# Performance work log

Measured on AMD Instinct MI355X. Metric: run time of the kernel, lower is better.

The kernel has to match this reference:

```python
import jax, jax.numpy as jnp
import numpy as np

N_QUBITS = 12
N_LAYERS = 3


def _apply_ry(state, theta, q):
    # state: (2,)*n real statevector; RY on qubit q
    c = jnp.cos(theta * 0.5)
    s = jnp.sin(theta * 0.5)
    st = jnp.moveaxis(state, q, 0)
    st = jnp.stack([c * st[0] - s * st[1], s * st[0] + c * st[1]])
    return jnp.moveaxis(st, 0, q)


def _apply_cz(state, q, r):
    st = jnp.moveaxis(state, (q, r), (0, 1))
    st = st.at[1, 1].multiply(-1.0)
    return jnp.moveaxis(st, (0, 1), (q, r))


def _embed(x, params):
    # angle-embedding ansatz: L layers of RY(theta[l,q]+x[q]) + CZ ring
    n = N_QUBITS
    state = jnp.zeros((2,) * n, dtype=x.dtype).at[(0,) * n].set(1.0)
    for l in range(N_LAYERS):
        for q in range(n):
            state = _apply_ry(state, params[l, q] + x[q], q)
        for q in range(n):
            state = _apply_cz(state, q, (q + 1) % n)
    return state.reshape(-1)  # (2^n,)


def setup_inputs() -> dict:
    key = jax.random.key(0)
    k1, k2, k3 = jax.random.split(key, 3)
    data = jax.random.uniform(k1, (2048, N_QUBITS), dtype=jnp.float32)
    labels = jax.random.randint(k2, (2048,), 0, 2, dtype=jnp.int32)
    params = jax.random.normal(k3, (N_LAYERS, N_QUBITS), dtype=jnp.float32)
    return {"data": data, "labels": labels, "params": params}


def reference(data, labels, params):
    # Psi[i] = U(x_i, params)|0>, k_ij = |<psi_j|psi_i>|^2 (== prob of amp 0 of U^dag(x_j)U(x_i)|0>)
    psi = jax.vmap(_embed, in_axes=(0, None))(data, params)  # (N, 2^n)
    K = jnp.square(psi @ psi.T)                              # (N, N) pairwise kernel
    lab = 2.0 * labels.astype(psi.dtype) - 1.0               # {0,1} -> {-1,+1}
    LL = jnp.outer(lab, lab)
    kernel_polarity = jnp.sum(LL * K)
    square_sum_k = jnp.sum(K * K)
    square_sum_l = jnp.sum(LL * LL)
    return kernel_polarity / jnp.sqrt(square_sum_k * square_sum_l)
```

## Files before the change

### kernel.cpp

```cpp
#include <hip/hip_runtime.h>
#include <math.h>

#define NQ    12
#define DIM   4096
#define K_EXT 8192
#define KSL   1024
#define NSAMP 2048
#define NLAY  3
#define NT2   16
#define NTRI2 136
#define NSLICE 8
#define BK    64

typedef __attribute__((ext_vector_type(8)))  short bf16x8;
typedef __attribute__((ext_vector_type(16))) float floatx16;

__device__ __forceinline__ unsigned short f32_to_bf16(float x) {
    unsigned u = __builtin_bit_cast(unsigned, x);
    u += 0x7FFFu + ((u >> 16) & 1u);
    return (unsigned short)(u >> 16);
}
__device__ __forceinline__ float bf16_to_f32(unsigned short h) {
    unsigned u = (unsigned)h << 16;
    return __builtin_bit_cast(float, u);
}

__device__ __forceinline__ void gl_lds16(const unsigned short* g, unsigned short* l) {
    __builtin_amdgcn_global_load_lds(
        (const __attribute__((address_space(1))) unsigned int*)g,
        (__attribute__((address_space(3))) unsigned int*)l,
        16, 0, 0);
}

__device__ __forceinline__ void tri_decode(int bid, int& bi, int& bj) {
    int i = (int)((33.0 - sqrt(33.0*33.0 - 8.0*(double)bid)) * 0.5);
    int start = i*(33-i)/2;
    while (bid < start)               { --i; start = i*(33-i)/2; }
    while (bid >= start + (NT2 - i))  { start += NT2 - i; ++i; }
    bi = i; bj = i + (bid - start);
}

__global__ __launch_bounds__(256) void sim_kernel(const float* __restrict__ data,
                                                  const float* __restrict__ params,
                                                  unsigned short* __restrict__ pe)
{
    __shared__ float CS[2*36], SN[2*36];
    __shared__ float ex[2][128*33];
    const int tid  = threadIdx.x;
    const int wave = tid >> 6, lane = tid & 63;
    const int sidx = wave >> 1;
    const int w    = wave & 1;
    const int smp  = blockIdx.x * 2 + sidx;

    if (w == 0 && lane < NLAY*NQ) {
        const int q = lane % NQ;
        const float th = 0.5f * (params[lane] + data[smp*NQ + q]);
        CS[sidx*36 + lane] = cosf(th);
        SN[sidx*36 + lane] = sinf(th);
    }
    __syncthreads();

    float v[32];
    #pragma unroll
    for (int r = 0; r < 32; ++r) v[r] = 0.f;
    if (w == 0 && lane == 0) v[0] = 1.f;

    const int P5 = __popc(lane & (lane >> 1) & 0x1F) & 1;
    const int l0 = lane & 1, l5 = (lane >> 5) & 1;
    const int base = P5 ^ (l5 & w);
    const float fA0 = base             ? -1.f : 1.f;
    const float fA1 = (base ^ w)       ? -1.f : 1.f;
    const float fB0 = (base ^ l0)      ? -1.f : 1.f;
    const float fB1 = (base ^ l0 ^ w)  ? -1.f : 1.f;

    float*       exw = &ex[sidx][(w*64       + lane)*33];
    const float* exp_ = &ex[sidx][((1-w)*64  + lane)*33];

    #pragma unroll 1
    for (int l = 0; l < NLAY; ++l) {
        const float* cs = &CS[sidx*36 + l*NQ];
        const float* sn = &SN[sidx*36 + l*NQ];
        #pragma unroll
        for (int b = 0; b < 5; ++b) {
            const float c = cs[b], s = sn[b];
            const int M = 1 << b;
            #pragma unroll
            for (int r = 0; r < 32; ++r) {
                if (!(r & M)) {
                    const float a0 = v[r], a1 = v[r | M];
                    v[r]     = c * a0 - s * a1;
                    v[r | M] = s * a0 + c * a1;
                }
            }
        }
        {
            const float c0 = cs[5], s0 = sn[5];
            const float t0 = (lane & 1) ? s0 : -s0;
            #pragma unroll
            for (int r = 0; r < 32; ++r) {
                const int iv = __builtin_bit_cast(int, v[r]);
                const int pv = __builtin_amdgcn_update_dpp(0, iv, 0xB1, 0xF, 0xF, true);
                v[r] = c0 * v[r] + t0 * __builtin_bit_cast(float, pv);
            }
            const float c1 = cs[6], s1 = sn[6];
            const float t1 = (lane & 2) ? s1 : -s1;
            #pragma unroll
            for (int r = 0; r < 32; ++r) {
                const int iv = __builtin_bit_cast(int, v[r]);
                const int pv = __builtin_amdgcn_update_dpp(0, iv, 0x4E, 0xF, 0xF, true);
                v[r] = c1 * v[r] + t1 * __builtin_bit_cast(float, pv);
            }
        }
        #pragma unroll 1
        for (int q = 7; q < 11; ++q) {
            const float c = cs[q], s = sn[q];
            const int   lb = q - 5;
            const float t = ((lane >> lb) & 1) ? s : -s;
            const int   m = 1 << lb;
            #pragma unroll
            for (int r = 0; r < 32; ++r) {
                const float p = __shfl_xor(v[r], m, 64);
                v[r] = c * v[r] + t * p;
            }
        }
        {
            const float c = cs[11], s = sn[11];
            const float t = w ? s : -s;
            __syncthreads();
            #pragma unroll
            for (int r = 0; r < 32; ++r) exw[r] = v[r];
            __syncthreads();
            #pragma unroll
            for (int r = 0; r < 32; ++r) v[r] = c * v[r] + t * exp_[r];
        }
        #pragma unroll
        for (int r = 0; r < 32; ++r) {
            const int P4 = __popc(r & (r >> 1) & 0xF) & 1;
            const int r0 = r & 1, r4 = (r >> 4) & 1;
            float f = r4 ? (r0 ? fB1 : fB0) : (r0 ? fA1 : fA0);
            if (P4) f = -f;
            v[r] *= f;
        }
    }

    const int sw = smp & 7;
    const int ell = w*64 + lane;
    unsigned short* outb = pe + (size_t)smp * K_EXT;
    #pragma unroll
    for (int c = 0; c < 4; ++c) {
        uint4 H, L;
        {
            const float x0 = v[c*8+0], x1 = v[c*8+1];
            const unsigned short h0 = f32_to_bf16(x0), h1 = f32_to_bf16(x1);
            H.x = (unsigned)h0 | ((unsigned)h1 << 16);
            L.x = (unsigned)f32_to_bf16(x0 - bf16_to_f32(h0)) |
                  ((unsigned)f32_to_bf16(x1 - bf16_to_f32(h1)) << 16);
        }
        {
            const float x0 = v[c*8+2], x1 = v[c*8+3];
            const unsigned short h0 = f32_to_bf16(x0), h1 = f32_to_bf16(x1);
            H.y = (unsigned)h0 | ((unsigned)h1 << 16);
            L.y = (unsigned)f32_to_bf16(x0 - bf16_to_f32(h0)) |
                  ((unsigned)f32_to_bf16(x1 - bf16_to_f32(h1)) << 16);
        }
        {
            const float x0 = v[c*8+4], x1 = v[c*8+5];
            const unsigned short h0 = f32_to_bf16(x0), h1 = f32_to_bf16(x1);
            H.z = (unsigned)h0 | ((unsigned)h1 << 16);
            L.z = (unsigned)f32_to_bf16(x0 - bf16_to_f32(h0)) |
                  ((unsigned)f32_to_bf16(x1 - bf16_to_f32(h1)) << 16);
        }
        {
            const float x0 = v[c*8+6], x1 = v[c*8+7];
            const unsigned short h0 = f32_to_bf16(x0), h1 = f32_to_bf16(x1);
            H.w = (unsigned)h0 | ((unsigned)h1 << 16);
            L.w = (unsigned)f32_to_bf16(x0 - bf16_to_f32(h0)) |
                  ((unsigned)f32_to_bf16(x1 - bf16_to_f32(h1)) << 16);
        }
        const int gc  = 4*ell + c;
        const int pos = (gc & ~7) | ((gc ^ sw) & 7);
        *(uint4*)&outb[pos*8]       = H;
        *(uint4*)&outb[DIM + pos*8] = L;
    }
}

__global__ __launch_bounds__(256) void gram_partial(const unsigned short* __restrict__ pe,
                                                    float* __restrict__ Gp)
{
    __shared__ __align__(16) unsigned short stage[2*128*64];

    unsigned short* As = stage;
    unsigned short* Bs = stage + 128*64;

    const int tid   = threadIdx.x;
    const int tile  = blockIdx.x >> 3;
    const int slice = blockIdx.x & 7;
    int bi, bj; tri_decode(tile, bi, bj);
    const int k0 = slice * KSL;

    const int wave = tid >> 6, lane = tid & 63;
    const int qr = (wave >> 1) * 64;
    const int qc = (wave &  1) * 64;
    const int mrow = lane & 31;
    const int chsel = lane >> 5;
    const int sw = mrow & 7;

    floatx16 c00, c01, c10, c11;
    #pragma unroll
    for (int i = 0; i < 16; ++i) { c00[i]=0.f; c01[i]=0.f; c10[i]=0.f; c11[i]=0.f; }

    const int mat  = wave >> 1;
    const int half = wave & 1;
    const unsigned short* gbase = pe
        + ((size_t)((mat ? bj : bi)*128 + half*64 + (lane >> 3))) * K_EXT
        + k0 + (lane & 7)*8;
    unsigned short* lbase = (mat ? Bs : As) + half*64*64;

    for (int kk = 0; kk < KSL; kk += BK) {
        __syncthreads();
        const unsigned short* g = gbase + kk;
        #pragma unroll
        for (int i = 0; i < 8; ++i)
            gl_lds16(g + (size_t)i*8*K_EXT, lbase + i*512);
        __syncthreads();

        #pragma unroll
        for (int ks = 0; ks < 4; ++ks) {
            const int ch = (ks*2 + chsel) ^ sw;
            const bf16x8 a0 = *(const bf16x8*)&As[(qr +      mrow)*64 + ch*8];
            const bf16x8 a1 = *(const bf16x8*)&As[(qr + 32 + mrow)*64 + ch*8];
            const bf16x8 b0 = *(const bf16x8*)&Bs[(qc +      mrow)*64 + ch*8];
            const bf16x8 b1 = *(const bf16x8*)&Bs[(qc + 32 + mrow)*64 + ch*8];
            c00 = __builtin_amdgcn_mfma_f32_32x32x16_bf16(a0, b0, c00, 0, 0, 0);
            c01 = __builtin_amdgcn_mfma_f32_32x32x16_bf16(a0, b1, c01, 0, 0, 0);
            c10 = __builtin_amdgcn_mfma_f32_32x32x16_bf16(a1, b0, c10, 0, 0, 0);
            c11 = __builtin_amdgcn_mfma_f32_32x32x16_bf16(a1, b1, c11, 0, 0, 0);
        }
    }

    float* Gt = Gp + ((size_t)slice * NTRI2 + tile) * 16384;
    const int crow = chsel * 4;
    const int ccol = lane & 31;
    #pragma unroll
    for (int rr = 0; rr < 16; ++rr) {
        const int rl = (rr & 3) + 8*(rr >> 2) + crow;
        const int r0 = qr + rl,  r1 = qr + 32 + rl;
        const int cA = qc + ccol, cB = qc + 32 + ccol;
        Gt[r0*128 + cA] = c00[rr];
        Gt[r0*128 + cB] = c01[rr];
        Gt[r1*128 + cA] = c10[rr];
        Gt[r1*128 + cB] = c11[rr];
    }
}

__global__ __launch_bounds__(256) void gram_reduce(const float* __restrict__ Gp,
                                                   const int* __restrict__ labels,
                                                   double* __restrict__ part1,
                                                   double* __restrict__ part2)
{
    __shared__ float la[128], lb[128];
    __shared__ double red[256];
    const int tid  = threadIdx.x;
    const int tile = blockIdx.x >> 2;
    const int quar = blockIdx.x & 3;
    int bi, bj; tri_decode(tile, bi, bj);

    if (tid < 128) la[tid]       = 2.0f*(float)labels[bi*128 + tid]       - 1.0f;
    else           lb[tid - 128] = 2.0f*(float)labels[bj*128 + tid - 128] - 1.0f;
    __syncthreads();

    const size_t stride = (size_t)NTRI2 * 16384;
    const float* g0 = Gp + (size_t)tile * 16384 + quar * 4096;

    double s1 = 0.0, s2 = 0.0;
    #pragma unroll 2
    for (int u = 0; u < 16; ++u) {
        const int e  = u*256 + tid;
        const int ge = quar*4096 + e;
        float g = 0.f;
        #pragma unroll
        for (int s = 0; s < NSLICE; ++s) g += g0[e + (size_t)s*stride];
        const int row = ge >> 7, col = ge & 127;
        const float w = (bi < bj) ? 2.0f : ((row < col) ? 2.0f : ((row == col) ? 1.0f : 0.0f));
        const float g2 = g * g;
        s1 += (double)(w * la[row] * lb[col] * g2);
        const double d = (double)g2;
        s2 += (double)w * d * d;
    }

    red[tid] = s1; __syncthreads();
    for (int off = 128; off; off >>= 1) { if (tid < off) red[tid] += red[tid+off]; __syncthreads(); }
    if (tid == 0) part1[blockIdx.x] = red[0];
    __syncthreads();
    red[tid] = s2; __syncthreads();
    for (int off = 128; off; off >>= 1) { if (tid < off) red[tid] += red[tid+off]; __syncthreads(); }
    if (tid == 0) part2[blockIdx.x] = red[0];
}

__global__ __launch_bounds__(256) void finalize_kernel(const double* __restrict__ part1,
                                                       const double* __restrict__ part2,
                                                       float* __restrict__ out)
{
    __shared__ double r1[256], r2[256];
    const int tid = threadIdx.x;
    double a = 0.0, b = 0.0;
    #pragma unroll
    for (int u = 0; u < 3; ++u) {
        const int s = tid + u*256;
        if (s < NTRI2*4) { a += part1[s]; b += part2[s]; }
    }
    r1[tid] = a; r2[tid] = b; __syncthreads();
    for (int off = 128; off; off >>= 1) {
        if (tid < off) { r1[tid] += r1[tid+off]; r2[tid] += r2[tid+off]; }
        __syncthreads();
    }
    if (tid == 0) out[0] = (float)(r1[0] / (sqrt(r2[0]) * (double)NSAMP));
}

extern "C" void kernel_launch(void* const* d_in, const int* in_sizes, int n_in,
                              void* d_out, int out_size, void* d_ws, size_t ws_size,
                              hipStream_t stream)
{
    const float* data   = (const float*)d_in[0];
    const int*   labels = (const int*)d_in[1];
    const float* params = (const float*)d_in[2];

    double* part1 = (double*)d_ws;
    double* part2 = part1 + 768;
    unsigned short* psi_ext = (unsigned short*)((char*)d_ws + 16384);
    float* Gp = (float*)((char*)d_ws + 16384 + (size_t)NSAMP*K_EXT*2);

    sim_kernel<<<NSAMP/2, 256, 0, stream>>>(data, params, psi_ext);
    gram_partial<<<NTRI2*NSLICE, 256, 0, stream>>>(psi_ext, Gp);
    gram_reduce<<<NTRI2*4, 256, 0, stream>>>(Gp, labels, part1, part2);
    finalize_kernel<<<1, 256, 0, stream>>>(part1, part2, (float*)d_out);
}
```

Baseline: 154.9 us.

## Replace shuffle gates with LDS transpose alternating register/lane qubit mapping

Each layer now applies five qubits in registers, two via DPP, then does one shared-memory transpose so another five qubits become register-local, instead of four cross-lane shuffles per element plus an exchange for qubit 11. The qubit-to-register mapping alternates between even and odd layers, and the CZ phase is computed per element from popcount parity and applied via sign-bit XOR. This targets the cost of the many ds_bpermute shuffles, in exchange for a larger LDS buffer and the risk of bank conflicts or mapping errors in the final layout used by the store.

```diff
diff --git a/kernel.cpp b/kernel.cpp
--- a/kernel.cpp
+++ b/kernel.cpp
@@ -45,7 +45,7 @@
                                                   unsigned short* __restrict__ pe)
 {
     __shared__ float CS[2*36], SN[2*36];
-    __shared__ float ex[2][128*33];
+    __shared__ float trans[2][4608];
     const int tid  = threadIdx.x;
     const int wave = tid >> 6, lane = tid & 63;
     const int sidx = wave >> 1;
@@ -65,36 +65,34 @@
     for (int r = 0; r < 32; ++r) v[r] = 0.f;
     if (w == 0 && lane == 0) v[0] = 1.f;
 
-    const int P5 = __popc(lane & (lane >> 1) & 0x1F) & 1;
-    const int l0 = lane & 1, l5 = (lane >> 5) & 1;
-    const int base = P5 ^ (l5 & w);
-    const float fA0 = base             ? -1.f : 1.f;
-    const float fA1 = (base ^ w)       ? -1.f : 1.f;
-    const float fB0 = (base ^ l0)      ? -1.f : 1.f;
-    const float fB1 = (base ^ l0 ^ w)  ? -1.f : 1.f;
-
-    float*       exw = &ex[sidx][(w*64       + lane)*33];
-    const float* exp_ = &ex[sidx][((1-w)*64  + lane)*33];
+    float* buf = trans[sidx];
+    float* wb  = buf + 36*lane + 2304*w;
+    const float* rb = buf + ((lane>>2)&15) + 16*w + 36*(lane&3);
 
     #pragma unroll 1
     for (int l = 0; l < NLAY; ++l) {
         const float* cs = &CS[sidx*36 + l*NQ];
         const float* sn = &SN[sidx*36 + l*NQ];
-        #pragma unroll
-        for (int b = 0; b < 5; ++b) {
-            const float c = cs[b], s = sn[b];
-            const int M = 1 << b;
-            #pragma unroll
-            for (int r = 0; r < 32; ++r) {
-                if (!(r & M)) {
-                    const float a0 = v[r], a1 = v[r | M];
-                    v[r]     = c * a0 - s * a1;
-                    v[r | M] = s * a0 + c * a1;
+        const int even = !(l & 1);
+
+        {
+            const int qb = even ? 7 : 2;
+            #pragma unroll
+            for (int b = 0; b < 5; ++b) {
+                const float c = cs[qb + b], s = sn[qb + b];
+                const int M = 1 << b;
+                #pragma unroll
+                for (int r = 0; r < 32; ++r) {
+                    if (!(r & M)) {
+                        const float a0 = v[r], a1 = v[r | M];
+                        v[r]     = c * a0 - s * a1;
+                        v[r | M] = s * a0 + c * a1;
+                    }
                 }
             }
         }
         {
-            const float c0 = cs[5], s0 = sn[5];
+            const float c0 = cs[0], s0 = sn[0];
             const float t0 = (lane & 1) ? s0 : -s0;
             #pragma unroll
             for (int r = 0; r < 32; ++r) {
@@ -102,7 +100,7 @@
                 const int pv = __builtin_amdgcn_update_dpp(0, iv, 0xB1, 0xF, 0xF, true);
                 v[r] = c0 * v[r] + t0 * __builtin_bit_cast(float, pv);
             }
-            const float c1 = cs[6], s1 = sn[6];
+            const float c1 = cs[1], s1 = sn[1];
             const float t1 = (lane & 2) ? s1 : -s1;
             #pragma unroll
             for (int r = 0; r < 32; ++r) {
@@ -111,35 +109,45 @@
                 v[r] = c1 * v[r] + t1 * __builtin_bit_cast(float, pv);
             }
         }
-        #pragma unroll 1
-        for (int q = 7; q < 11; ++q) {
-            const float c = cs[q], s = sn[q];
-            const int   lb = q - 5;
-            const float t = ((lane >> lb) & 1) ? s : -s;
-            const int   m = 1 << lb;
+        __syncthreads();
+        #pragma unroll
+        for (int t = 0; t < 8; ++t) {
+            float4 q4;
+            q4.x = v[4*t]; q4.y = v[4*t+1]; q4.z = v[4*t+2]; q4.w = v[4*t+3];
+            *(float4*)&wb[4*t] = q4;
+        }
+        __syncthreads();
+        #pragma unroll
+        for (int r = 0; r < 32; ++r)
+            v[r] = rb[144*(r & 15) + 2304*(r >> 4)];
+
+        {
+            const int qb = even ? 2 : 7;
+            #pragma unroll
+            for (int b = 0; b < 5; ++b) {
+                const float c = cs[qb + b], s = sn[qb + b];
+                const int M = 1 << b;
+                #pragma unroll
+                for (int r = 0; r < 32; ++r) {
+                    if (!(r & M)) {
+                        const float a0 = v[r], a1 = v[r | M];
+                        v[r]     = c * a0 - s * a1;
+                        v[r | M] = s * a0 + c * a1;
+                    }
+                }
+            }
+        }
+        {
+            const int Base = even ? ((lane & 3) | (((lane >> 2) & 15) << 7) | (w << 11))
+                                  : (lane | (w << 6));
+            const int shift = even ? 2 : 7;
             #pragma unroll
             for (int r = 0; r < 32; ++r) {
-                const float p = __shfl_xor(v[r], m, 64);
-                v[r] = c * v[r] + t * p;
-            }
-        }
-        {
-            const float c = cs[11], s = sn[11];
-            const float t = w ? s : -s;
-            __syncthreads();
-            #pragma unroll
-            for (int r = 0; r < 32; ++r) exw[r] = v[r];
-            __syncthreads();
-            #pragma unroll
-            for (int r = 0; r < 32; ++r) v[r] = c * v[r] + t * exp_[r];
-        }
-        #pragma unroll
-        for (int r = 0; r < 32; ++r) {
-            const int P4 = __popc(r & (r >> 1) & 0xF) & 1;
-            const int r0 = r & 1, r4 = (r >> 4) & 1;
-            float f = r4 ? (r0 ? fB1 : fB0) : (r0 ? fA1 : fA0);
-            if (P4) f = -f;
-            v[r] *= f;
+                const int i  = Base | (r << shift);
+                const int t  = ((i >> 1) | (i << 11)) & 0xFFF;
+                const int p  = __popc(i & t) & 1;
+                v[r] = __builtin_bit_cast(float, __builtin_bit_cast(int, v[r]) ^ (p << 31));
+            }
         }
     }
 
```

Result: faster. 147.3 us (-4.9%).
